# Kernel optimization log

Hardware: AMD Instinct MI355X
Metric: run time of the kernel (lower is better)

## Reference

```python
import jax, jax.numpy as jnp
import numpy as np


def _calculate_iou(b1, b2):
    # b1, b2: (N, 4) with x, y, w, h
    b1x1, b1y1 = b1[:, 0], b1[:, 1]
    b1x2, b1y2 = b1[:, 0] + b1[:, 2], b1[:, 1] + b1[:, 3]
    b2x1, b2y1 = b2[:, 0], b2[:, 1]
    b2x2, b2y2 = b2[:, 0] + b2[:, 2], b2[:, 1] + b2[:, 3]
    areas1 = (b1x2 - b1x1) * (b1y2 - b1y1)
    areas2 = (b2x2 - b2x1) * (b2y2 - b2y1)
    iw = jnp.clip(jnp.minimum(b1x2, b2x2) - jnp.maximum(b1x1, b2x1), 0.0)
    ih = jnp.clip(jnp.minimum(b1y2, b2y2) - jnp.maximum(b1y1, b2y1), 0.0)
    inter = iw * ih
    return inter / (areas1 + areas2 - inter)


NUM_CLASSES = 80
OUT_W, OUT_H = 13, 13


def _build_target_one(bbox_pred_s, bbox_gt_s, cls_gt_s, anchors):
    # bbox_pred_s: (hw, A, 4); bbox_gt_s: (nb, 4); cls_gt_s: (nb,)
    hw, A = bbox_pred_s.shape[0], bbox_pred_s.shape[1]
    # anchor aspect-ratio matching
    ra = anchors[:, 0] / anchors[:, 1]                      # (A,)
    rg = bbox_gt_s[:, 2] / bbox_gt_s[:, 3]                  # (nb,)
    best = jnp.argmin(jnp.abs(ra[:, None] - rg[None, :]), axis=0)  # (nb,)
    cx = bbox_gt_s[:, 0] * OUT_W
    cy = bbox_gt_s[:, 1] * OUT_H
    cell = (jnp.floor(cy) * OUT_W + jnp.floor(cx)).astype(jnp.int32)  # (nb,)
    tx = cx - jnp.floor(cx)
    ty = cy - jnp.floor(cy)
    tgt_xywh = jnp.stack([tx, ty, jnp.sqrt(bbox_gt_s[:, 2]), jnp.sqrt(bbox_gt_s[:, 3])], axis=-1)
    bbox_built = jnp.zeros((hw, A, 4), bbox_pred_s.dtype).at[cell, best].set(tgt_xywh)
    bbox_mask = jnp.zeros((hw, A, 1), bbox_pred_s.dtype).at[cell, best].set(1.0)
    cls_built = jnp.zeros((hw, A, NUM_CLASSES), bbox_pred_s.dtype).at[cell, best, cls_gt_s].set(1.0)
    cls_mask = jnp.zeros((hw, A, 1), bbox_pred_s.dtype).at[cell, best].set(1.0)
    iou_mask = jnp.full((hw, A, 1), 0.5, bbox_pred_s.dtype).at[cell, best].set(1.0)
    iou_built = _calculate_iou(bbox_pred_s.reshape(-1, 4), bbox_built.reshape(-1, 4)).reshape(hw, A, 1)
    return bbox_built, iou_built, cls_built, bbox_mask, iou_mask, cls_mask


def _forward(bbox_pred, iou_pred, prob_pred, bbox_gt, cls_gt, anchors):
    # apply anchors: w,h -> sqrt(w*aw), sqrt(h*ah)
    aw = anchors[:, 0][:, None]  # (A,1) broadcasts over (B,hw,A,1)
    ah = anchors[:, 1][:, None]
    bp = jnp.concatenate([
        bbox_pred[..., :2],
        jnp.sqrt(bbox_pred[..., 2:3] * aw),
        jnp.sqrt(bbox_pred[..., 3:4] * ah),
    ], axis=-1)
    targets = jax.vmap(_build_target_one, in_axes=(0, 0, 0, None))(bp, bbox_gt, cls_gt, anchors)
    bbox_built, iou_built, cls_built, bbox_mask, iou_mask, cls_mask = [
        jax.lax.stop_gradient(t) for t in targets
    ]
    mse = lambda a, b: jnp.mean((a - b) ** 2)
    bbox_loss = mse(bp * bbox_mask, bbox_built * bbox_mask)
    iou_loss = mse(iou_pred * iou_mask, iou_built * iou_mask)
    cls_loss = mse(prob_pred * cls_mask, cls_built * cls_mask)
    return bbox_loss * 5.0 + iou_loss + cls_loss


def setup_inputs() -> dict:
    key = jax.random.key(0)
    k1, k2, k3, k4, k5 = jax.random.split(key, 5)
    B, HW, A, C, NB = 512, OUT_W * OUT_H, 5, NUM_CLASSES, 20
    bbox_pred = jax.random.uniform(k1, (B, HW, A, 4), jnp.float32, 1e-3, 1.0)
    iou_pred = jax.random.uniform(k2, (B, HW, A, 1), jnp.float32)
    prob_pred = jax.random.uniform(k3, (B, HW, A, C), jnp.float32)
    bbox_gt = jax.random.uniform(k4, (B, NB, 4), jnp.float32, 1e-3, 1.0 - 1e-3)
    cls_gt = jax.random.randint(k5, (B, NB), 0, C, jnp.int32)
    anchors = jnp.array([
        [1.3221, 1.73145], [3.19275, 4.00944], [5.05587, 8.09892],
        [9.47112, 4.84053], [11.2364, 10.0071]], jnp.float32)
    return {"bbox_pred": bbox_pred, "iou_pred": iou_pred, "prob_pred": prob_pred,
            "bbox_gt": bbox_gt, "cls_gt": cls_gt, "anchors": anchors}


def reference(bbox_pred, iou_pred, prob_pred, bbox_gt, cls_gt, anchors):
    return _forward(bbox_pred, iou_pred, prob_pred, bbox_gt, cls_gt, anchors)
```

## Files before the change

### kernel.cpp

```cpp
#include <hip/hip_runtime.h>

#define NUM_CLASSES 80
#define OUT_W 13
#define OUT_H 13
#define HW (OUT_W * OUT_H)
#define NA 5
#define NB 20
#define NBATCH 512

__global__ __launch_bounds__(256)
void yolo_loss_main(const float* __restrict__ bbox_pred,
                    const float* __restrict__ iou_pred,
                    const float* __restrict__ prob_pred,
                    const float* __restrict__ bbox_gt,
                    const int*   __restrict__ cls_gt,
                    const float* __restrict__ anchors,
                    double* __restrict__ partials)
{
    const int b   = blockIdx.x;
    const int tid = threadIdx.x;

    __shared__ float s_anch[NA * 2];
    __shared__ int   s_slot[NB];
    __shared__ int   s_cls[NB];
    __shared__ float s_tgt[NB][4];
    __shared__ int   s_win[NB];
    __shared__ int   s_dup[NB];
    __shared__ double s_red[3][4];

    if (tid < NA * 2) s_anch[tid] = anchors[tid];

    float gx = 0.f, gy = 0.f, gw = 0.f, gh = 0.f;
    float ra0 = 0.f, ra1 = 0.f, ra2 = 0.f, ra3 = 0.f, ra4 = 0.f;
    int   my_cls = 0;
    if (tid < NB) {
        const float* g = bbox_gt + ((size_t)b * NB + tid) * 4;
        gx = g[0]; gy = g[1]; gw = g[2]; gh = g[3];
        my_cls = cls_gt[(size_t)b * NB + tid];
        ra0 = anchors[0] / anchors[1];
        ra1 = anchors[2] / anchors[3];
        ra2 = anchors[4] / anchors[5];
        ra3 = anchors[6] / anchors[7];
        ra4 = anchors[8] / anchors[9];
    }

    double bbox_acc = 0.0, iou_acc = 0.0, cls_acc = 0.0;
    const float* ip = iou_pred + (size_t)b * HW * NA;
    for (int i = tid; i < HW * NA; i += 256) {
        const float p = ip[i];
        iou_acc += (double)(0.25f * p * p);
    }

    if (tid < NB) {
        const float rg = gw / gh;
        int best = 0;
        float bd = fabsf(ra0 - rg);
        float d;
        d = fabsf(ra1 - rg); if (d < bd) { bd = d; best = 1; }
        d = fabsf(ra2 - rg); if (d < bd) { bd = d; best = 2; }
        d = fabsf(ra3 - rg); if (d < bd) { bd = d; best = 3; }
        d = fabsf(ra4 - rg); if (d < bd) { bd = d; best = 4; }
        const float cx = gx * (float)OUT_W;
        const float cy = gy * (float)OUT_H;
        const float fx = floorf(cx), fy = floorf(cy);
        const int cell = (int)(fy * (float)OUT_W + fx);
        s_slot[tid]   = cell * NA + best;
        s_cls[tid]    = my_cls;
        s_tgt[tid][0] = cx - fx;
        s_tgt[tid][1] = cy - fy;
        s_tgt[tid][2] = sqrtf(gw);
        s_tgt[tid][3] = sqrtf(gh);
    }
    __syncthreads();

    if (tid < NB) {
        const int n = tid, slot = s_slot[n];
        int win = 1;
        for (int m = n + 1; m < NB; ++m)
            if (s_slot[m] == slot) { win = 0; break; }
        s_win[n] = win;
        int dup = 0;
        for (int m = 0; m < n; ++m)
            if (s_slot[m] == slot && s_cls[m] == s_cls[n]) { dup = 1; break; }
        s_dup[n] = dup;
    }
    __syncthreads();

    if (tid < NB && s_win[tid]) {
        const int n = tid;
        const int slot = s_slot[n];
        const int a = slot % NA;
        const float aw = s_anch[2 * a], ah = s_anch[2 * a + 1];
        const float* pp = bbox_pred + (((size_t)b * HW * NA) + slot) * 4;
        const float bp0 = pp[0], bp1 = pp[1];
        const float bp2 = sqrtf(pp[2] * aw);
        const float bp3 = sqrtf(pp[3] * ah);
        const float t0 = s_tgt[n][0], t1 = s_tgt[n][1];
        const float t2 = s_tgt[n][2], t3 = s_tgt[n][3];

        const float d0 = bp0 - t0, d1 = bp1 - t1, d2 = bp2 - t2, d3 = bp3 - t3;
        bbox_acc += (double)(d0 * d0) + (double)(d1 * d1)
                  + (double)(d2 * d2) + (double)(d3 * d3);

        const float area1 = bp2 * bp3, area2 = t2 * t3;
        float iw = fminf(bp0 + bp2, t0 + t2) - fmaxf(bp0, t0);
        float ih = fminf(bp1 + bp3, t1 + t3) - fmaxf(bp1, t1);
        iw = fmaxf(iw, 0.0f);
        ih = fmaxf(ih, 0.0f);
        const float inter = iw * ih;
        const float iou = inter / (area1 + area2 - inter);

        const float p = ip[slot];
        iou_acc += (double)((p - iou) * (p - iou) - 0.25f * p * p);
    }

    const float* prp = prob_pred + (size_t)b * HW * NA * NUM_CLASSES;
    for (int idx = tid; idx < NB * NUM_CLASSES; idx += 256) {
        const int n = idx / NUM_CLASSES, c = idx - n * NUM_CLASSES;
        if (s_win[n]) {
            const float p = prp[(size_t)s_slot[n] * NUM_CLASSES + c];
            cls_acc += (double)(p * p);
        }
    }
    if (tid < NB && !s_dup[tid]) {
        const float p = prp[(size_t)s_slot[tid] * NUM_CLASSES + s_cls[tid]];
        cls_acc += (double)(1.0f - 2.0f * p);
    }

    for (int off = 32; off > 0; off >>= 1) {
        bbox_acc += __shfl_down(bbox_acc, off);
        iou_acc  += __shfl_down(iou_acc,  off);
        cls_acc  += __shfl_down(cls_acc,  off);
    }
    const int wave = tid >> 6, lane = tid & 63;
    if (lane == 0) {
        s_red[0][wave] = bbox_acc;
        s_red[1][wave] = iou_acc;
        s_red[2][wave] = cls_acc;
    }
    __syncthreads();
    if (tid == 0) {
        double bs = 0.0, is = 0.0, cs = 0.0;
        for (int w = 0; w < 4; ++w) { bs += s_red[0][w]; is += s_red[1][w]; cs += s_red[2][w]; }
        const double N1 = (double)NBATCH * HW * NA * 4;
        const double N2 = (double)NBATCH * HW * NA;
        const double N3 = (double)NBATCH * HW * NA * NUM_CLASSES;
        partials[b] = 5.0 * bs / N1 + is / N2 + cs / N3;
    }
}

__global__ __launch_bounds__(256)
void yolo_loss_final(const double* __restrict__ partials,
                     float* __restrict__ out)
{
    const int tid = threadIdx.x;
    __shared__ double s_red[4];

    double sum = partials[tid] + partials[tid + 256];
    for (int off = 32; off > 0; off >>= 1)
        sum += __shfl_down(sum, off);
    const int wave = tid >> 6, lane = tid & 63;
    if (lane == 0) s_red[wave] = sum;
    __syncthreads();
    if (tid == 0)
        out[0] = (float)(s_red[0] + s_red[1] + s_red[2] + s_red[3]);
}

extern "C" void kernel_launch(void* const* d_in, const int* in_sizes, int n_in,
                              void* d_out, int out_size, void* d_ws, size_t ws_size,
                              hipStream_t stream)
{
    const float* bbox_pred = (const float*)d_in[0];
    const float* iou_pred  = (const float*)d_in[1];
    const float* prob_pred = (const float*)d_in[2];
    const float* bbox_gt   = (const float*)d_in[3];
    const int*   cls_gt    = (const int*)d_in[4];
    const float* anchors   = (const float*)d_in[5];
    float* out = (float*)d_out;
    double* partials = (double*)d_ws;

    yolo_loss_main<<<NBATCH, 256, 0, stream>>>(bbox_pred, iou_pred, prob_pred,
                                               bbox_gt, cls_gt, anchors, partials);
    yolo_loss_final<<<1, 256, 0, stream>>>(partials, out);
}
```

Before: 15.23 us.

## Vectorize loads, merge loss accumulators, use wave barrier, shrink final reduction

Anchors are kept in registers instead of shared memory, and the gt, bbox and class-probability reads become float4 loads. The three per-thread double accumulators are scaled and merged into one before the shuffle reduction, which cuts shuffle traffic. The first __syncthreads is replaced by a wave barrier, which is valid because all NB threads are in wave 0. The final kernel uses a single 64-thread wave with no shared memory. The kernel is already tiny and latency-bound, so these micro-savings are small, and the reordered summation changes floating-point rounding slightly.

```diff
diff --git a/kernel.cpp b/kernel.cpp
--- a/kernel.cpp
+++ b/kernel.cpp
@@ -20,46 +20,44 @@
     const int b   = blockIdx.x;
     const int tid = threadIdx.x;
 
-    __shared__ float s_anch[NA * 2];
     __shared__ int   s_slot[NB];
     __shared__ int   s_cls[NB];
     __shared__ float s_tgt[NB][4];
     __shared__ int   s_win[NB];
     __shared__ int   s_dup[NB];
-    __shared__ double s_red[3][4];
-
-    if (tid < NA * 2) s_anch[tid] = anchors[tid];
+    __shared__ double s_red[4];
 
     float gx = 0.f, gy = 0.f, gw = 0.f, gh = 0.f;
-    float ra0 = 0.f, ra1 = 0.f, ra2 = 0.f, ra3 = 0.f, ra4 = 0.f;
+    float a0w=0.f,a0h=0.f,a1w=0.f,a1h=0.f,a2w=0.f,a2h=0.f,a3w=0.f,a3h=0.f,a4w=0.f,a4h=0.f;
     int   my_cls = 0;
     if (tid < NB) {
-        const float* g = bbox_gt + ((size_t)b * NB + tid) * 4;
-        gx = g[0]; gy = g[1]; gw = g[2]; gh = g[3];
+        const float4 g4 = *(const float4*)(bbox_gt + ((size_t)b * NB + tid) * 4);
+        gx = g4.x; gy = g4.y; gw = g4.z; gh = g4.w;
         my_cls = cls_gt[(size_t)b * NB + tid];
-        ra0 = anchors[0] / anchors[1];
-        ra1 = anchors[2] / anchors[3];
-        ra2 = anchors[4] / anchors[5];
-        ra3 = anchors[6] / anchors[7];
-        ra4 = anchors[8] / anchors[9];
+        a0w = anchors[0]; a0h = anchors[1];
+        a1w = anchors[2]; a1h = anchors[3];
+        a2w = anchors[4]; a2h = anchors[5];
+        a3w = anchors[6]; a3h = anchors[7];
+        a4w = anchors[8]; a4h = anchors[9];
     }
 
-    double bbox_acc = 0.0, iou_acc = 0.0, cls_acc = 0.0;
+    double acc_iou = 0.0;
+    double w = 0.0;
     const float* ip = iou_pred + (size_t)b * HW * NA;
     for (int i = tid; i < HW * NA; i += 256) {
         const float p = ip[i];
-        iou_acc += (double)(0.25f * p * p);
+        acc_iou += (double)(0.25f * p * p);
     }
 
     if (tid < NB) {
         const float rg = gw / gh;
         int best = 0;
-        float bd = fabsf(ra0 - rg);
+        float bd = fabsf(a0w / a0h - rg);
         float d;
-        d = fabsf(ra1 - rg); if (d < bd) { bd = d; best = 1; }
-        d = fabsf(ra2 - rg); if (d < bd) { bd = d; best = 2; }
-        d = fabsf(ra3 - rg); if (d < bd) { bd = d; best = 3; }
-        d = fabsf(ra4 - rg); if (d < bd) { bd = d; best = 4; }
+        d = fabsf(a1w / a1h - rg); if (d < bd) { bd = d; best = 1; }
+        d = fabsf(a2w / a2h - rg); if (d < bd) { bd = d; best = 2; }
+        d = fabsf(a3w / a3h - rg); if (d < bd) { bd = d; best = 3; }
+        d = fabsf(a4w / a4h - rg); if (d < bd) { bd = d; best = 4; }
         const float cx = gx * (float)OUT_W;
         const float cy = gy * (float)OUT_H;
         const float fx = floorf(cx), fy = floorf(cy);
@@ -71,8 +69,7 @@
         s_tgt[tid][2] = sqrtf(gw);
         s_tgt[tid][3] = sqrtf(gh);
     }
-    __syncthreads();
-
+    __builtin_amdgcn_wave_barrier();
     if (tid < NB) {
         const int n = tid, slot = s_slot[n];
         int win = 1;
@@ -86,21 +83,29 @@
     }
     __syncthreads();
 
+    const double N1 = (double)NBATCH * HW * NA * 4;
+    const double N2 = (double)NBATCH * HW * NA;
+    const double N3 = (double)NBATCH * HW * NA * NUM_CLASSES;
+
     if (tid < NB && s_win[tid]) {
         const int n = tid;
         const int slot = s_slot[n];
         const int a = slot % NA;
-        const float aw = s_anch[2 * a], ah = s_anch[2 * a + 1];
-        const float* pp = bbox_pred + (((size_t)b * HW * NA) + slot) * 4;
-        const float bp0 = pp[0], bp1 = pp[1];
-        const float bp2 = sqrtf(pp[2] * aw);
-        const float bp3 = sqrtf(pp[3] * ah);
+        float aw = a0w, ah = a0h;
+        if (a == 1) { aw = a1w; ah = a1h; }
+        if (a == 2) { aw = a2w; ah = a2h; }
+        if (a == 3) { aw = a3w; ah = a3h; }
+        if (a == 4) { aw = a4w; ah = a4h; }
+        const float4 pp = *(const float4*)(bbox_pred + (((size_t)b * HW * NA) + slot) * 4);
+        const float bp0 = pp.x, bp1 = pp.y;
+        const float bp2 = sqrtf(pp.z * aw);
+        const float bp3 = sqrtf(pp.w * ah);
         const float t0 = s_tgt[n][0], t1 = s_tgt[n][1];
         const float t2 = s_tgt[n][2], t3 = s_tgt[n][3];
 
         const float d0 = bp0 - t0, d1 = bp1 - t1, d2 = bp2 - t2, d3 = bp3 - t3;
-        bbox_acc += (double)(d0 * d0) + (double)(d1 * d1)
-                  + (double)(d2 * d2) + (double)(d3 * d3);
+        w += 5.0 / N1 * ((double)(d0 * d0) + (double)(d1 * d1)
+                       + (double)(d2 * d2) + (double)(d3 * d3));
 
         const float area1 = bp2 * bp3, area2 = t2 * t3;
         float iw = fminf(bp0 + bp2, t0 + t2) - fmaxf(bp0, t0);
@@ -111,59 +116,46 @@
         const float iou = inter / (area1 + area2 - inter);
 
         const float p = ip[slot];
-        iou_acc += (double)((p - iou) * (p - iou) - 0.25f * p * p);
+        acc_iou += (double)((p - iou) * (p - iou) - 0.25f * p * p);
     }
 
     const float* prp = prob_pred + (size_t)b * HW * NA * NUM_CLASSES;
-    for (int idx = tid; idx < NB * NUM_CLASSES; idx += 256) {
-        const int n = idx / NUM_CLASSES, c = idx - n * NUM_CLASSES;
+    double acc_cls = 0.0;
+    for (int idx = tid; idx < NB * (NUM_CLASSES / 4); idx += 256) {
+        const int n = idx / (NUM_CLASSES / 4), q = idx - n * (NUM_CLASSES / 4);
         if (s_win[n]) {
-            const float p = prp[(size_t)s_slot[n] * NUM_CLASSES + c];
-            cls_acc += (double)(p * p);
+            const float4 p4 = *(const float4*)(prp + (size_t)s_slot[n] * NUM_CLASSES + q * 4);
+            acc_cls += (double)(p4.x * p4.x) + (double)(p4.y * p4.y)
+                     + (double)(p4.z * p4.z) + (double)(p4.w * p4.w);
         }
     }
     if (tid < NB && !s_dup[tid]) {
         const float p = prp[(size_t)s_slot[tid] * NUM_CLASSES + s_cls[tid]];
-        cls_acc += (double)(1.0f - 2.0f * p);
+        acc_cls += (double)(1.0f - 2.0f * p);
     }
 
-    for (int off = 32; off > 0; off >>= 1) {
-        bbox_acc += __shfl_down(bbox_acc, off);
-        iou_acc  += __shfl_down(iou_acc,  off);
-        cls_acc  += __shfl_down(cls_acc,  off);
-    }
+    w += acc_iou / N2 + acc_cls / N3;
+    for (int off = 32; off > 0; off >>= 1)
+        w += __shfl_down(w, off);
     const int wave = tid >> 6, lane = tid & 63;
-    if (lane == 0) {
-        s_red[0][wave] = bbox_acc;
-        s_red[1][wave] = iou_acc;
-        s_red[2][wave] = cls_acc;
-    }
+    if (lane == 0) s_red[wave] = w;
     __syncthreads();
-    if (tid == 0) {
-        double bs = 0.0, is = 0.0, cs = 0.0;
-        for (int w = 0; w < 4; ++w) { bs += s_red[0][w]; is += s_red[1][w]; cs += s_red[2][w]; }
-        const double N1 = (double)NBATCH * HW * NA * 4;
-        const double N2 = (double)NBATCH * HW * NA;
-        const double N3 = (double)NBATCH * HW * NA * NUM_CLASSES;
-        partials[b] = 5.0 * bs / N1 + is / N2 + cs / N3;
-    }
+    if (tid == 0)
+        partials[b] = s_red[0] + s_red[1] + s_red[2] + s_red[3];
 }
 
-__global__ __launch_bounds__(256)
+__global__ __launch_bounds__(64)
 void yolo_loss_final(const double* __restrict__ partials,
                      float* __restrict__ out)
 {
     const int tid = threadIdx.x;
-    __shared__ double s_red[4];
-
-    double sum = partials[tid] + partials[tid + 256];
+    double s = 0.0;
+    #pragma unroll
+    for (int k = 0; k < 8; ++k)
+        s += partials[tid + 64 * k];
     for (int off = 32; off > 0; off >>= 1)
-        sum += __shfl_down(sum, off);
-    const int wave = tid >> 6, lane = tid & 63;
-    if (lane == 0) s_red[wave] = sum;
-    __syncthreads();
-    if (tid == 0)
-        out[0] = (float)(s_red[0] + s_red[1] + s_red[2] + s_red[3]);
+        s += __shfl_down(s, off);
+    if (tid == 0) out[0] = (float)s;
 }
 
 extern "C" void kernel_launch(void* const* d_in, const int* in_sizes, int n_in,
@@ -181,5 +173,5 @@
 
     yolo_loss_main<<<NBATCH, 256, 0, stream>>>(bbox_pred, iou_pred, prob_pred,
                                                bbox_gt, cls_gt, anchors, partials);
-    yolo_loss_final<<<1, 256, 0, stream>>>(partials, out);
+    yolo_loss_final<<<1, 64, 0, stream>>>(partials, out);
 }
```

Result: faster. 13.53 us (-11.1%).
